# Performance work log

Measured on AMD Instinct MI355X. Metric: run time of the kernel, lower is better.

## Reference

```python
import jax, jax.numpy as jnp
import numpy as np

B, H, L, D_QK, D_V, M = 4, 16, 4096, 64, 64, 256
EPS = 1e-6


def _gaussian_orf(key, m, d):
    """Structured Gaussian orthogonal random features (SORF), as in gaussian_orf."""
    num_squares = m // d + 1
    keys = jax.random.split(key, num_squares)
    blocks = jax.vmap(lambda k: jnp.linalg.qr(jax.random.normal(k, (d, d)))[0].T)(keys)
    b = blocks.reshape(-1, d)[:m]
    return jnp.sqrt(d) * b  # structured multiplier sqrt(d)*I


def setup_inputs() -> dict:
    key = jax.random.key(0)
    kq, kk, kv, kp = jax.random.split(key, 4)
    qs = jax.random.normal(kq, (B, H, L, D_QK), dtype=jnp.float32)
    ks = jax.random.normal(kk, (B, H, L, D_QK), dtype=jnp.float32)
    vs = jax.random.normal(kv, (B, H, L, D_V), dtype=jnp.float32)
    mask = jnp.ones((B, L), dtype=jnp.float32)
    proj = _gaussian_orf(kp, M, D_QK).astype(jnp.float32)
    return {"qs": qs, "ks": ks, "vs": vs, "mask": mask, "proj": proj}


def _phi(x, proj):
    """Stable positive softmax kernel: exp(x @ Omega^T - |x|^2/2) / sqrt(m)."""
    m = proj.shape[0]
    x_proj = jnp.einsum('bld,md->blm', x, proj)
    half_sq_norm = 0.5 * jnp.square(x).sum(-1, keepdims=True)
    return jnp.exp(x_proj - half_sq_norm) / jnp.sqrt(m)


def reference(qs, ks, vs, mask, proj):
    b, h, q_len, d_qk = qs.shape
    # (B H L D) -> ((B H) L D)
    qs_f = qs.reshape(b * h, q_len, d_qk)
    ks_f = ks.reshape(b * h, ks.shape[2], d_qk)
    vs_f = vs.reshape(b * h, vs.shape[2], vs.shape[3])
    normalizer = 1.0 / jnp.power(jnp.float32(d_qk), 0.25)
    qs_prime = _phi(qs_f * normalizer, proj)          # (BH, Q, M)
    ks_prime = _phi(ks_f * normalizer, proj)          # (BH, K, M)
    ks_prime = ks_prime * jnp.repeat(mask, h, axis=0)[..., None]
    # fast_attend: linear attention matmul chain
    c = jnp.concatenate([vs_f, jnp.ones((*vs_f.shape[:-1], 1), vs_f.dtype)], axis=-1)  # (BH, K, Dv+1)
    buf_1 = jnp.einsum('bkm,bke->bme', ks_prime, c)   # (BH, M, Dv+1)
    buf_2 = jnp.einsum('bqm,bme->bqe', qs_prime, buf_1)
    num, den = buf_2[..., :-1], buf_2[..., -1]
    den = jnp.where(den < EPS, EPS, den)
    ctx = num / den[..., None]
    return ctx.reshape(b, h, q_len, -1)
```

## Files before the change

### kernel.cpp

```cpp
#include <hip/hip_runtime.h>
#include <hip/hip_bf16.h>

#define Lq    4096
#define NORM  0.3535533905932738f
#define SC    0.0625f
#define EPSV  1e-6f
#define EPSV16 1.6e-5f

typedef short short8 __attribute__((ext_vector_type(8)));
typedef short short4v __attribute__((ext_vector_type(4)));
typedef float float4v __attribute__((ext_vector_type(4)));

#define MFMA16(a, b, c) __builtin_amdgcn_mfma_f32_16x16x32_bf16(a, b, c, 0, 0, 0)

__device__ __forceinline__ short f2bf(float f) {
  unsigned u = __builtin_bit_cast(unsigned, f);
  unsigned r = (u + 0x7FFFu + ((u >> 16) & 1u)) >> 16;
  return (short)r;
}

#define PITCH 80
#define P2    268
#define PP    68
#define PB    260

#define BUF1_FLOATS ((size_t)64 * 256 * 80)
#define BUF1T_OFF   (BUF1_FLOATS * 4)
#define PROJB_OFF   (BUF1T_OFF + (size_t)64 * 20480 * 2)

__global__ __launch_bounds__(256)
void k0_proj(const float* __restrict__ proj, short* __restrict__ projb) {
  int i = (blockIdx.x * 256 + threadIdx.x) * 4;
  float4 v = *reinterpret_cast<const float4*>(proj + i);
  short4v o; o[0] = f2bf(v.x); o[1] = f2bf(v.y); o[2] = f2bf(v.z); o[3] = f2bf(v.w);
  *reinterpret_cast<short4v*>(projb + i) = o;
}

__global__ __launch_bounds__(256, 2)
void k1_build(const float* __restrict__ ks, const float* __restrict__ vs,
              const float* __restrict__ mask, const short* __restrict__ projb,
              float* __restrict__ buf1) {
  __shared__ short lx[64 * PITCH];
  __shared__ short lvT[80 * PITCH];
  __shared__ short lphiT[256 * PITCH];
  __shared__ float lhnp[64 * 16];
  __shared__ float lhn[64];
  __shared__ float lmfAll[512];

  const int t    = threadIdx.x;
  const int w    = t >> 6;
  const int lane = t & 63;
  const int c    = lane & 15;
  const int quad = lane >> 4;
  const int chunk = blockIdx.x;
  const int bh    = blockIdx.y;
  const int bidx  = bh >> 4;

  for (int i = t; i < 512; i += 256)
    lmfAll[i] = mask[(size_t)bidx * Lq + chunk * 512 + i] * SC;

  short8 pf[4][2];
#pragma unroll
  for (int nt = 0; nt < 4; ++nt)
#pragma unroll
    for (int h = 0; h < 2; ++h)
      pf[nt][h] = *reinterpret_cast<const short8*>(
          &projb[(size_t)(w * 64 + nt * 16 + c) * 64 + h * 32 + quad * 8]);

#pragma unroll
  for (int i = 0; i < 4; ++i) {
    int idx = i * 256 + t;
    int row = 64 + (idx >> 6), col = idx & 63;
    lvT[row * PITCH + col] = (row == 64) ? (short)0x3F80 : (short)0;
  }

  float4v acc[4][5];
#pragma unroll
  for (int mt = 0; mt < 4; ++mt)
#pragma unroll
    for (int nt = 0; nt < 5; ++nt) acc[mt][nt] = (float4v){0.f, 0.f, 0.f, 0.f};

  const float4* ks4 = reinterpret_cast<const float4*>(ks);
  const float4* vs4 = reinterpret_cast<const float4*>(vs);
  const int key0 = (t >> 4);
  const int d4   = t & 15;

  float4 kx[4], vx[4];
#pragma unroll
  for (int i = 0; i < 4; ++i) {
    size_t base = ((size_t)bh * Lq + chunk * 512 + (i * 16 + key0)) * 16 + d4;
    kx[i] = ks4[base]; vx[i] = vs4[base];
  }

  for (int kt = 0; kt < 8; ++kt) {
    __syncthreads();

#pragma unroll
    for (int i = 0; i < 4; ++i) {
      int key = i * 16 + key0;
      float4 v = kx[i];
      v.x *= NORM; v.y *= NORM; v.z *= NORM; v.w *= NORM;
      lhnp[key * 16 + d4] = v.x * v.x + v.y * v.y + v.z * v.z + v.w * v.w;
      short4v o; o[0] = f2bf(v.x); o[1] = f2bf(v.y); o[2] = f2bf(v.z); o[3] = f2bf(v.w);
      *reinterpret_cast<short4v*>(&lx[key * PITCH + d4 * 4]) = o;
      float4 u = vx[i];
      lvT[(d4 * 4 + 0) * PITCH + key] = f2bf(u.x);
      lvT[(d4 * 4 + 1) * PITCH + key] = f2bf(u.y);
      lvT[(d4 * 4 + 2) * PITCH + key] = f2bf(u.z);
      lvT[(d4 * 4 + 3) * PITCH + key] = f2bf(u.w);
    }
    __syncthreads();

    if (kt + 1 < 8) {
#pragma unroll
      for (int i = 0; i < 4; ++i) {
        size_t base = ((size_t)bh * Lq + chunk * 512 + (kt + 1) * 64 + (i * 16 + key0)) * 16 + d4;
        kx[i] = ks4[base]; vx[i] = vs4[base];
      }
    }
    if (t < 64) {
      float s = 0.f;
#pragma unroll
      for (int j = 0; j < 16; ++j) s += lhnp[t * 16 + j];
      lhn[t] = 0.5f * s;
    }
    __syncthreads();

#pragma unroll
    for (int mt = 0; mt < 4; ++mt) {
      short8 a0 = *reinterpret_cast<short8*>(&lx[(mt * 16 + c) * PITCH + quad * 8]);
      short8 a1 = *reinterpret_cast<short8*>(&lx[(mt * 16 + c) * PITCH + 32 + quad * 8]);
      float4v hn4 = *reinterpret_cast<float4v*>(&lhn[mt * 16 + quad * 4]);
      float4v mf4 = *reinterpret_cast<float4v*>(&lmfAll[kt * 64 + mt * 16 + quad * 4]);
#pragma unroll
      for (int nt = 0; nt < 4; ++nt) {
        float4v p = (float4v){0.f, 0.f, 0.f, 0.f};
        p = MFMA16(a0, pf[nt][0], p);
        p = MFMA16(a1, pf[nt][1], p);
        short4v ph;
#pragma unroll
        for (int r = 0; r < 4; ++r)
          ph[r] = f2bf(__expf(p[r] - hn4[r]) * mf4[r]);
        *reinterpret_cast<short4v*>(
            &lphiT[(w * 64 + nt * 16 + c) * PITCH + mt * 16 + quad * 4]) = ph;
      }
    }

    short8 bv[5][2];
#pragma unroll
    for (int nt = 0; nt < 5; ++nt) {
      bv[nt][0] = *reinterpret_cast<short8*>(&lvT[(nt * 16 + c) * PITCH + quad * 8]);
      bv[nt][1] = *reinterpret_cast<short8*>(&lvT[(nt * 16 + c) * PITCH + 32 + quad * 8]);
    }
#pragma unroll
    for (int mt = 0; mt < 4; ++mt) {
      short8 a0 = *reinterpret_cast<short8*>(&lphiT[(w * 64 + mt * 16 + c) * PITCH + quad * 8]);
      short8 a1 = *reinterpret_cast<short8*>(&lphiT[(w * 64 + mt * 16 + c) * PITCH + 32 + quad * 8]);
#pragma unroll
      for (int nt = 0; nt < 5; ++nt) {
        acc[mt][nt] = MFMA16(a0, bv[nt][0], acc[mt][nt]);
        acc[mt][nt] = MFMA16(a1, bv[nt][1], acc[mt][nt]);
      }
    }
  }

  float* bp = buf1 + (size_t)bh * 256 * 80;
#pragma unroll
  for (int mt = 0; mt < 4; ++mt)
#pragma unroll
    for (int nt = 0; nt < 5; ++nt)
#pragma unroll
      for (int r = 0; r < 4; ++r) {
        int feat = w * 64 + mt * 16 + quad * 4 + r;
        int e    = nt * 16 + c;
        atomicAdd(bp + (size_t)feat * 80 + e, acc[mt][nt][r]);
      }
}

__global__ __launch_bounds__(256, 8)
void k1_reduce(const float* __restrict__ buf1, short* __restrict__ buf1T) {
  const int bh = blockIdx.x;
  const int s  = blockIdx.y;
  const int t  = threadIdx.x;
#pragma unroll
  for (int j = 0; j < 10; ++j) {
    int idx = s * 2560 + j * 256 + t;
    int e = idx >> 8, feat = idx & 255;
    buf1T[(size_t)bh * 20480 + idx] = f2bf(buf1[(size_t)bh * 20480 + feat * 80 + e]);
  }
}

__global__ __launch_bounds__(512, 1)
void k2_ctx(const float* __restrict__ qs, const short* __restrict__ projb,
            const short* __restrict__ buf1T, float* __restrict__ out) {
  __shared__ short lproj[256 * PP];
  __shared__ short lbT[64 * PB];
  __shared__ short lden[256];
  __shared__ short lphi[128 * P2];
  __shared__ float lhnw[128];

  const int t    = threadIdx.x;
  const int w    = t >> 6;
  const int lane = t & 63;
  const int c    = lane & 15;
  const int quad = lane >> 4;
  const int q0   = blockIdx.x * 128;
  const int bhb  = blockIdx.y * 8;

#pragma unroll
  for (int i = 0; i < 4; ++i) {
    int idx = i * 512 + t;
    int row = idx >> 3, col = (idx & 7) * 8;
    *reinterpret_cast<short8*>(&lproj[row * PP + col]) =
        *reinterpret_cast<const short8*>(&projb[(size_t)row * 64 + col]);
  }
  {
    const short* bT = buf1T + (size_t)bhb * 20480;
#pragma unroll
    for (int i = 0; i < 4; ++i) {
      int idx = i * 512 + t;
      int e = idx >> 5, f = (idx & 31) * 8;
      *reinterpret_cast<short8*>(&lbT[e * PB + f]) =
          *reinterpret_cast<const short8*>(&bT[e * 256 + f]);
    }
    if (t < 32)
      *reinterpret_cast<short8*>(&lden[t * 8]) =
          *reinterpret_cast<const short8*>(&bT[16384 + t * 8]);
  }
  const float* qrow0 = qs + ((size_t)bhb * Lq + q0 + w * 16 + c) * 64;
  float4 v0 = *reinterpret_cast<const float4*>(qrow0 + quad * 8);
  float4 v1 = *reinterpret_cast<const float4*>(qrow0 + quad * 8 + 4);
  float4 v2 = *reinterpret_cast<const float4*>(qrow0 + 32 + quad * 8);
  float4 v3 = *reinterpret_cast<const float4*>(qrow0 + 32 + quad * 8 + 4);
  __syncthreads();

  for (int it = 0; it < 8; ++it) {
    const int bh = bhb + it;

    short8 nb[4]; short8 nden; float4 n0, n1, n2, n3;
    if (it < 7) {
      const short* bTn = buf1T + (size_t)(bh + 1) * 20480;
#pragma unroll
      for (int i = 0; i < 4; ++i) {
        int idx = i * 512 + t;
        int e = idx >> 5, f = (idx & 31) * 8;
        nb[i] = *reinterpret_cast<const short8*>(&bTn[e * 256 + f]);
      }
      if (t < 32) nden = *reinterpret_cast<const short8*>(&bTn[16384 + t * 8]);
      const float* qn = qs + ((size_t)(bh + 1) * Lq + q0 + w * 16 + c) * 64;
      n0 = *reinterpret_cast<const float4*>(qn + quad * 8);
      n1 = *reinterpret_cast<const float4*>(qn + quad * 8 + 4);
      n2 = *reinterpret_cast<const float4*>(qn + 32 + quad * 8);
      n3 = *reinterpret_cast<const float4*>(qn + 32 + quad * 8 + 4);
    }

    v0.x *= NORM; v0.y *= NORM; v0.z *= NORM; v0.w *= NORM;
    v1.x *= NORM; v1.y *= NORM; v1.z *= NORM; v1.w *= NORM;
    v2.x *= NORM; v2.y *= NORM; v2.z *= NORM; v2.w *= NORM;
    v3.x *= NORM; v3.y *= NORM; v3.z *= NORM; v3.w *= NORM;

    float s = v0.x * v0.x + v0.y * v0.y + v0.z * v0.z + v0.w * v0.w
            + v1.x * v1.x + v1.y * v1.y + v1.z * v1.z + v1.w * v1.w
            + v2.x * v2.x + v2.y * v2.y + v2.z * v2.z + v2.w * v2.w
            + v3.x * v3.x + v3.y * v3.y + v3.z * v3.z + v3.w * v3.w;
    s += __shfl_xor(s, 16);
    s += __shfl_xor(s, 32);
    if (quad == 0) lhnw[w * 16 + c] = 0.5f * s;

    short8 qa0, qa1;
    qa0[0] = f2bf(v0.x); qa0[1] = f2bf(v0.y); qa0[2] = f2bf(v0.z); qa0[3] = f2bf(v0.w);
    qa0[4] = f2bf(v1.x); qa0[5] = f2bf(v1.y); qa0[6] = f2bf(v1.z); qa0[7] = f2bf(v1.w);
    qa1[0] = f2bf(v2.x); qa1[1] = f2bf(v2.y); qa1[2] = f2bf(v2.z); qa1[3] = f2bf(v2.w);
    qa1[4] = f2bf(v3.x); qa1[5] = f2bf(v3.y); qa1[6] = f2bf(v3.z); qa1[7] = f2bf(v3.w);

    float4v hn4 = *reinterpret_cast<float4v*>(&lhnw[w * 16 + quad * 4]);

#pragma unroll
    for (int nt = 0; nt < 16; ++nt) {
      short8 b0 = *reinterpret_cast<short8*>(&lproj[(nt * 16 + c) * PP + quad * 8]);
      short8 b1 = *reinterpret_cast<short8*>(&lproj[(nt * 16 + c) * PP + 32 + quad * 8]);
      float4v p = (float4v){0.f, 0.f, 0.f, 0.f};
      p = MFMA16(qa0, b0, p);
      p = MFMA16(qa1, b1, p);
#pragma unroll
      for (int r = 0; r < 4; ++r)
        lphi[(w * 16 + quad * 4 + r) * P2 + nt * 16 + c] =
            f2bf(__expf(p[r] - hn4[r]));
    }

    __syncthreads();

    float4v cacc[5];
#pragma unroll
    for (int nt = 0; nt < 5; ++nt) cacc[nt] = (float4v){0.f, 0.f, 0.f, 0.f};
#pragma unroll
    for (int k2i = 0; k2i < 8; ++k2i) {
      short8 a = *reinterpret_cast<short8*>(&lphi[(w * 16 + c) * P2 + k2i * 32 + quad * 8]);
#pragma unroll
      for (int nt = 0; nt < 4; ++nt) {
        short8 b = *reinterpret_cast<short8*>(
            &lbT[(nt * 16 + c) * PB + k2i * 32 + quad * 8]);
        cacc[nt] = MFMA16(a, b, cacc[nt]);
      }
      short8 bd;
      if (c == 0) bd = *reinterpret_cast<short8*>(&lden[k2i * 32 + quad * 8]);
      else        bd = (short8){0, 0, 0, 0, 0, 0, 0, 0};
      cacc[4] = MFMA16(a, bd, cacc[4]);
    }

    float rinv[4];
#pragma unroll
    for (int r = 0; r < 4; ++r) {
      float den = __shfl(cacc[4][r], (lane & 48));
      den = fmaxf(den, EPSV16);
      rinv[r] = 1.0f / den;
    }
#pragma unroll
    for (int nt = 0; nt < 4; ++nt)
#pragma unroll
      for (int r = 0; r < 4; ++r) {
        int q = q0 + w * 16 + quad * 4 + r;
        out[((size_t)bh * Lq + q) * 64 + nt * 16 + c] = cacc[nt][r] * rinv[r];
      }

    __syncthreads();

    if (it < 7) {
#pragma unroll
      for (int i = 0; i < 4; ++i) {
        int idx = i * 512 + t;
        int e = idx >> 5, f = (idx & 31) * 8;
        *reinterpret_cast<short8*>(&lbT[e * PB + f]) = nb[i];
      }
      if (t < 32) *reinterpret_cast<short8*>(&lden[t * 8]) = nden;
      v0 = n0; v1 = n1; v2 = n2; v3 = n3;
    }
  }
}

extern "C" void kernel_launch(void* const* d_in, const int* in_sizes, int n_in,
                              void* d_out, int out_size, void* d_ws, size_t ws_size,
                              hipStream_t stream) {
  const float* qs   = (const float*)d_in[0];
  const float* ks   = (const float*)d_in[1];
  const float* vs   = (const float*)d_in[2];
  const float* mask = (const float*)d_in[3];
  const float* proj = (const float*)d_in[4];
  float* out  = (float*)d_out;
  float* buf1 = (float*)d_ws;
  short* buf1T = (short*)((char*)d_ws + BUF1T_OFF);
  short* projb = (short*)((char*)d_ws + PROJB_OFF);

  (void)in_sizes; (void)n_in; (void)out_size; (void)ws_size;

  hipMemsetAsync(buf1, 0, BUF1_FLOATS * sizeof(float), stream);
  k0_proj<<<dim3(16), 256, 0, stream>>>(proj, projb);
  k1_build<<<dim3(8, 64), 256, 0, stream>>>(ks, vs, mask, projb, buf1);
  k1_reduce<<<dim3(64, 8), 256, 0, stream>>>(buf1, buf1T);
  k2_ctx<<<dim3(32, 8), 512, 0, stream>>>(qs, projb, buf1T, out);
}
```

Baseline: 287.1 us.

## Shuffle-reduce key norms, swizzle V transpose in LDS, raise MFMA priority

In k1_build, the per-key squared norm is now reduced with wave shuffles and written straight to lhn. This drops the lhnp scratch array, the serial 64-thread reduction and one __syncthreads per tile. The transposed V tile in LDS uses an XOR swizzle on 8-key groups, and PITCH grows from 80 to 88, to cut bank conflicts on the strided transpose stores and the short8 reads. The PV MFMA loop is wrapped in s_setprio to favour matrix issue. Costs are more LDS per block from the larger pitch, which may limit occupancy, and PITCH is a shared macro that may also be used by other kernels.

```diff
diff --git a/kernel.cpp b/kernel.cpp
--- a/kernel.cpp
+++ b/kernel.cpp
@@ -19,7 +19,7 @@
   return (short)r;
 }
 
-#define PITCH 80
+#define PITCH 88
 #define P2    268
 #define PP    68
 #define PB    260
@@ -43,7 +43,6 @@
   __shared__ short lx[64 * PITCH];
   __shared__ short lvT[80 * PITCH];
   __shared__ short lphiT[256 * PITCH];
-  __shared__ float lhnp[64 * 16];
   __shared__ float lhn[64];
   __shared__ float lmfAll[512];
 
@@ -100,16 +99,21 @@
       int key = i * 16 + key0;
       float4 v = kx[i];
       v.x *= NORM; v.y *= NORM; v.z *= NORM; v.w *= NORM;
-      lhnp[key * 16 + d4] = v.x * v.x + v.y * v.y + v.z * v.z + v.w * v.w;
+      float ss = v.x * v.x + v.y * v.y + v.z * v.z + v.w * v.w;
+      ss += __shfl_xor(ss, 1);
+      ss += __shfl_xor(ss, 2);
+      ss += __shfl_xor(ss, 4);
+      ss += __shfl_xor(ss, 8);
+      if (d4 == 0) lhn[key] = 0.5f * ss;
       short4v o; o[0] = f2bf(v.x); o[1] = f2bf(v.y); o[2] = f2bf(v.z); o[3] = f2bf(v.w);
       *reinterpret_cast<short4v*>(&lx[key * PITCH + d4 * 4]) = o;
       float4 u = vx[i];
-      lvT[(d4 * 4 + 0) * PITCH + key] = f2bf(u.x);
-      lvT[(d4 * 4 + 1) * PITCH + key] = f2bf(u.y);
-      lvT[(d4 * 4 + 2) * PITCH + key] = f2bf(u.z);
-      lvT[(d4 * 4 + 3) * PITCH + key] = f2bf(u.w);
-    }
-    __syncthreads();
+      int col = ((key >> 3) ^ (d4 & 7)) * 8 + (key & 7);
+      lvT[(d4 * 4 + 0) * PITCH + col] = f2bf(u.x);
+      lvT[(d4 * 4 + 1) * PITCH + col] = f2bf(u.y);
+      lvT[(d4 * 4 + 2) * PITCH + col] = f2bf(u.z);
+      lvT[(d4 * 4 + 3) * PITCH + col] = f2bf(u.w);
+    }
 
     if (kt + 1 < 8) {
 #pragma unroll
@@ -117,12 +121,6 @@
         size_t base = ((size_t)bh * Lq + chunk * 512 + (kt + 1) * 64 + (i * 16 + key0)) * 16 + d4;
         kx[i] = ks4[base]; vx[i] = vs4[base];
       }
-    }
-    if (t < 64) {
-      float s = 0.f;
-#pragma unroll
-      for (int j = 0; j < 16; ++j) s += lhnp[t * 16 + j];
-      lhn[t] = 0.5f * s;
     }
     __syncthreads();
 
@@ -149,9 +147,13 @@
     short8 bv[5][2];
 #pragma unroll
     for (int nt = 0; nt < 5; ++nt) {
-      bv[nt][0] = *reinterpret_cast<short8*>(&lvT[(nt * 16 + c) * PITCH + quad * 8]);
-      bv[nt][1] = *reinterpret_cast<short8*>(&lvT[(nt * 16 + c) * PITCH + 32 + quad * 8]);
-    }
+      int rsw = (nt * 4 + (c >> 2)) & 7;
+      bv[nt][0] = *reinterpret_cast<short8*>(
+          &lvT[(nt * 16 + c) * PITCH + ((0 + quad) ^ rsw) * 8]);
+      bv[nt][1] = *reinterpret_cast<short8*>(
+          &lvT[(nt * 16 + c) * PITCH + ((4 + quad) ^ rsw) * 8]);
+    }
+    __builtin_amdgcn_s_setprio(1);
 #pragma unroll
     for (int mt = 0; mt < 4; ++mt) {
       short8 a0 = *reinterpret_cast<short8*>(&lphiT[(w * 64 + mt * 16 + c) * PITCH + quad * 8]);
@@ -162,6 +164,7 @@
         acc[mt][nt] = MFMA16(a1, bv[nt][1], acc[mt][nt]);
       }
     }
+    __builtin_amdgcn_s_setprio(0);
   }
 
   float* bp = buf1 + (size_t)bh * 256 * 80;
```

After: 287.7 us. Within noise of the previous version (+0.2%).
